# Performance work log

Hardware: AMD Instinct MI355X
Metric: run time of the kernel (lower is better)

Reference implementation:

```python
import jax, jax.numpy as jnp
from jax import lax
import numpy as np


def setup_inputs() -> dict:
    key = jax.random.key(0)
    ks = jax.random.split(key, 7)
    B, C, L, H, K = 64, 256, 2048, 8, 3
    return {
        "src": jax.random.normal(ks[0], (B, C, L), dtype=jnp.float32),
        "conv_w": jax.random.normal(ks[1], (H, C, K), dtype=jnp.float32) * 0.05,
        "conv_b": jax.random.normal(ks[2], (H,), dtype=jnp.float32) * 0.05,
        "bn_gamma": jnp.ones((H,), dtype=jnp.float32),
        "bn_beta": jnp.zeros((H,), dtype=jnp.float32),
        "comb_w": jax.random.normal(ks[5], (H,), dtype=jnp.float32) * 0.3,
        "comb_b": jax.random.normal(ks[6], (1,), dtype=jnp.float32) * 0.05,
        "k": 64,
    }


def reference(src, conv_w, conv_b, bn_gamma, bn_beta, comb_w, comb_b, k):
    # src: (B, C, L); conv_w: (H, C, K)
    B, C, L = src.shape
    H, _, K = conv_w.shape
    # att_conv: valid 1D conv -> (B, H, Lp), Lp = L - K + 1
    xi = lax.conv_general_dilated(src, conv_w, (1,), 'VALID',
                                  dimension_numbers=('NCH', 'OIH', 'NCH'))
    xi = xi + conv_b[None, :, None]
    # BatchNorm1d in the original runs on a batch of 1 (training mode), so
    # stats are per-sample over the length dim; biased var, eps = 1e-5.
    mu = jnp.mean(xi, axis=2, keepdims=True)
    var = jnp.var(xi, axis=2, keepdims=True)
    xn = (xi - mu) * lax.rsqrt(var + 1e-5) * bn_gamma[None, :, None] + bn_beta[None, :, None]
    Lp = xn.shape[2]
    # per-(b, h) top-k indicator; indices are detached (.data) in the original
    _, idx = lax.top_k(xn, k)  # (B, H, k)
    bidx = jnp.arange(B)[:, None, None]
    hidx = jnp.arange(H)[None, :, None]
    ind = jnp.zeros_like(xn).at[bidx, hidx, idx].set(1.0)  # (B, H, Lp)
    m = jax.nn.sigmoid(xn) * ind  # softmask, (B, H, Lp)
    # kernel_size-way shifted-padding sum: M[b,h,l] = sum_i m[b,h,l-i] -> (B, H, L)
    M = sum(jnp.pad(m, ((0, 0), (0, 0), (i, K - 1 - i))) for i in range(K))
    # combine_conv is a 1x1 conv over heads; since softmasked_src[h,c,l] =
    # src[c,l] * M[h,l] / K, the head mix commutes with the src broadcast:
    gate = jnp.einsum('h,bhl->bl', comb_w, M) / K  # (B, L)
    return src * gate[:, None, :] + comb_b[0]  # (B, C, L)
```

## Files before the change

### kernel.cpp

```cpp
#include <hip/hip_runtime.h>
#include <hip/hip_bf16.h>

#define NB 64
#define NC 256
#define NL 2048
#define NH 8
#define KW 3
#define LP (NL - KW + 1)
#define NCHUNK 8
#define CPC (NC / NCHUNK)

typedef float v4f __attribute__((ext_vector_type(4)));

__device__ __forceinline__ unsigned fkey(float x) {
  unsigned b = __float_as_uint(x);
  return (b & 0x80000000u) ? ~b : (b | 0x80000000u);
}

__global__ __launch_bounds__(256) void conv_partial(
    const float* __restrict__ src, const float* __restrict__ conv_w,
    float* __restrict__ part) {
  const int t = threadIdx.x;
  const int lane = t & 63;
  const int l0 = blockIdx.x * 1024 + t * 4;
  const int b = blockIdx.y;
  const int cc = blockIdx.z;
  const int c0 = cc * CPC;

  float acc[NH][4];
#pragma unroll
  for (int h = 0; h < NH; ++h)
#pragma unroll
    for (int j = 0; j < 4; ++j) acc[h][j] = 0.f;

  const float* sp = src + ((size_t)b * NC + c0) * NL + l0;
  const bool tail = (lane == 63) && (l0 + 5 < NL);
#pragma unroll 2
  for (int c = 0; c < CPC; ++c) {
    v4f v = *(const v4f*)sp;
    float e0 = 0.f, e1 = 0.f;
    if (tail) { e0 = sp[4]; e1 = sp[5]; }
    sp += NL;
    float n0 = __shfl_down(v.x, 1);
    float n1 = __shfl_down(v.y, 1);
    if (lane == 63) { n0 = e0; n1 = e1; }
    float s0 = v.x, s1 = v.y, s2 = v.z, s3 = v.w, s4 = n0, s5 = n1;
#pragma unroll
    for (int h = 0; h < NH; ++h) {
      const float* w = conv_w + (h * NC + c0 + c) * KW;
      const float w0 = w[0], w1 = w[1], w2 = w[2];
      acc[h][0] = fmaf(s0, w0, fmaf(s1, w1, fmaf(s2, w2, acc[h][0])));
      acc[h][1] = fmaf(s1, w0, fmaf(s2, w1, fmaf(s3, w2, acc[h][1])));
      acc[h][2] = fmaf(s2, w0, fmaf(s3, w1, fmaf(s4, w2, acc[h][2])));
      acc[h][3] = fmaf(s3, w0, fmaf(s4, w1, fmaf(s5, w2, acc[h][3])));
    }
  }
#pragma unroll
  for (int h = 0; h < NH; ++h) {
    float* pr = part + ((size_t)(b * NH + h) * NCHUNK + cc) * NL + l0;
    if (l0 + 3 < LP) {
      *(v4f*)pr = *(v4f*)acc[h];
    } else {
#pragma unroll
      for (int j = 0; j < 4; ++j)
        if (l0 + j < LP) pr[j] = acc[h][j];
    }
  }
}

__global__ __launch_bounds__(256) void select_block(
    const float* __restrict__ part, float* __restrict__ xi,
    const float* __restrict__ conv_b, const float* __restrict__ bn_gamma,
    const float* __restrict__ bn_beta, const float* __restrict__ comb_w,
    const int* __restrict__ kptr) {
  const int t = threadIdx.x;
  const int lane = t & 63, wid = t >> 6;
  const int bh = blockIdx.x;
  const int h = bh & (NH - 1);
  __shared__ float xs[LP];
  __shared__ float smp[NL + 2];
  __shared__ int hist[256];
  __shared__ float rs[8];
  __shared__ float fbc[2];
  __shared__ int irs[8];
  __shared__ int ibc[4];

  const float cb = conv_b[h];
  const float* p0 = part + (size_t)bh * NCHUNK * NL;
  float s1 = 0.f, s2 = 0.f;
  for (int i = t; i < LP; i += 256) {
    float v0 = p0[i]           + p0[i + NL];
    float v1 = p0[i + 2 * NL]  + p0[i + 3 * NL];
    float v2 = p0[i + 4 * NL]  + p0[i + 5 * NL];
    float v3 = p0[i + 6 * NL]  + p0[i + 7 * NL];
    float v = ((v0 + v1) + (v2 + v3)) + cb;
    xs[i] = v;
    s1 += v;
    s2 += v * v;
  }
#pragma unroll
  for (int off = 32; off > 0; off >>= 1) {
    s1 += __shfl_down(s1, off);
    s2 += __shfl_down(s2, off);
  }
  if (lane == 0) { rs[wid] = s1; rs[wid + 4] = s2; }
  __syncthreads();
  if (t == 0) {
    float S = rs[0] + rs[1] + rs[2] + rs[3];
    float Q = rs[4] + rs[5] + rs[6] + rs[7];
    float mu = S / (float)LP;
    float var = Q / (float)LP - mu * mu;
    float inv = rsqrtf(var + 1e-5f);
    float sc = bn_gamma[h] * inv;
    fbc[0] = sc;
    fbc[1] = bn_beta[h] - mu * sc;
  }
  __syncthreads();
  {
    const float sc = fbc[0], sh = fbc[1];
    for (int i = t; i < LP; i += 256) xs[i] = fmaf(xs[i], sc, sh);
  }
  int kk = kptr[0];
  const int ktot = kk;
  unsigned prefix = 0, pm = 0;
  for (int pass = 0; pass < 4; ++pass) {
    const int shift = 24 - 8 * pass;
    hist[t] = 0;
    __syncthreads();
    for (int i = t; i < LP; i += 256) {
      unsigned u = fkey(xs[i]);
      if ((u & pm) == prefix) atomicAdd(&hist[(u >> shift) & 255], 1);
    }
    __syncthreads();
    if (t < 64) {
      const int h0 = hist[t * 4 + 0], h1 = hist[t * 4 + 1];
      const int h2 = hist[t * 4 + 2], h3 = hist[t * 4 + 3];
      const int g = h0 + h1 + h2 + h3;
      int sfx = g;
#pragma unroll
      for (int off = 1; off < 64; off <<= 1) {
        int o = __shfl(sfx, (t + off) & 63);
        if (t + off < 64) sfx += o;
      }
      const int A = sfx - g;
      const int s3 = A + h3, s2i = s3 + h2, s1i = s2i + h1, s0i = s1i + h0;
      int mybin = -1, mykk = 0;
      if (s0i >= kk && s0i - h0 < kk) { mybin = t * 4 + 0; mykk = kk - (s0i - h0); }
      if (s1i >= kk && s1i - h1 < kk) { mybin = t * 4 + 1; mykk = kk - (s1i - h1); }
      if (s2i >= kk && s2i - h2 < kk) { mybin = t * 4 + 2; mykk = kk - (s2i - h2); }
      if (s3  >= kk && s3  - h3 < kk) { mybin = t * 4 + 3; mykk = kk - (s3 - h3); }
      if (mybin >= 0) { ibc[0] = mybin; ibc[1] = mykk; }
    }
    __syncthreads();
    prefix |= ((unsigned)ibc[0]) << shift;
    pm |= 255u << shift;
    kk = ibc[1];
  }
  const unsigned T = prefix;

  int cgt = 0, ceq = 0;
  for (int i = t; i < LP; i += 256) {
    unsigned u = fkey(xs[i]);
    cgt += (u > T);
    ceq += (u == T);
  }
#pragma unroll
  for (int off = 32; off > 0; off >>= 1) {
    cgt += __shfl_down(cgt, off);
    ceq += __shfl_down(ceq, off);
  }
  if (lane == 0) { irs[wid] = cgt; irs[wid + 4] = ceq; }
  __syncthreads();
  if (t == 0) {
    ibc[2] = irs[0] + irs[1] + irs[2] + irs[3];
    ibc[3] = irs[4] + irs[5] + irs[6] + irs[7];
  }
  __syncthreads();
  const int need_eq = ktot - ibc[2];
  const bool tie = (ibc[3] != need_eq);

  for (int i = t; i < LP; i += 256) {
    float x = xs[i];
    unsigned u = fkey(x);
    bool sel = tie ? (u > T) : (u >= T);
    smp[i + 2] = sel ? 1.f / (1.f + __expf(-x)) : 0.f;
  }
  if (t < 2) { smp[t] = 0.f; smp[NL + t] = 0.f; }
  __syncthreads();
  if (tie && t == 0) {
    int taken = 0;
    for (int i = 0; i < LP && taken < need_eq; ++i) {
      float x = xs[i];
      if (fkey(x) == T) { smp[i + 2] = 1.f / (1.f + __expf(-x)); ++taken; }
    }
  }
  __syncthreads();

  const float cw = comb_w[h] * (1.0f / (float)KW);
  float* row = xi + (size_t)bh * NL;
  for (int l = t; l < NL; l += 256)
    row[l] = cw * ((smp[l + 2] + smp[l + 1]) + smp[l]);
}

__global__ __launch_bounds__(256) void scale_gate(
    const float* __restrict__ src, const float* __restrict__ xi,
    const float* __restrict__ comb_b, float* __restrict__ out) {
  const int t = threadIdx.x;
  const int cchunk = blockIdx.x >> 7;
  const int pairidx = (blockIdx.x & 127) * 256 + t;
  const int b = pairidx >> 9;
  const int l4 = pairidx & 511;
  const float cb = comb_b[0];

  const v4f* xp = (const v4f*)(xi + (size_t)b * NH * NL) + l4;
  v4f g = xp[0];
#pragma unroll
  for (int h = 1; h < NH; ++h) g += xp[(size_t)h * (NL / 4)];

  const int c0 = cchunk * (NC / 16);
  const v4f* sp = (const v4f*)src + ((size_t)b * NC + c0) * (NL / 4) + l4;
  v4f* op = (v4f*)out + ((size_t)b * NC + c0) * (NL / 4) + l4;
#pragma unroll 4
  for (int c = 0; c < NC / 16; ++c) {
    v4f sv = sp[(size_t)c * (NL / 4)];
    v4f ov;
    ov.x = fmaf(sv.x, g.x, cb);
    ov.y = fmaf(sv.y, g.y, cb);
    ov.z = fmaf(sv.z, g.z, cb);
    ov.w = fmaf(sv.w, g.w, cb);
    __builtin_nontemporal_store(ov, op + (size_t)c * (NL / 4));
  }
}

extern "C" void kernel_launch(void* const* d_in, const int* in_sizes, int n_in,
                              void* d_out, int out_size, void* d_ws, size_t ws_size,
                              hipStream_t stream) {
  const float* src = (const float*)d_in[0];
  const float* conv_w = (const float*)d_in[1];
  const float* conv_b = (const float*)d_in[2];
  const float* bn_gamma = (const float*)d_in[3];
  const float* bn_beta = (const float*)d_in[4];
  const float* comb_w = (const float*)d_in[5];
  const float* comb_b = (const float*)d_in[6];
  const int* kptr = (const int*)d_in[7];
  float* out = (float*)d_out;

  float* xi = (float*)d_ws;
  float* part = out;

  conv_partial<<<dim3(2, NB, NCHUNK), 256, 0, stream>>>(src, conv_w, part);
  select_block<<<NB * NH, 256, 0, stream>>>(part, xi, conv_b, bn_gamma,
                                            bn_beta, comb_w, kptr);
  scale_gate<<<2048, 256, 0, stream>>>(src, xi, comb_b, out);
}
```

Baseline: 92.67 us.

## Split conv reduction into more channel chunks and load halo via overlapping vectors

Doubles the number of channel chunks in the partial conv kernel, so twice as many blocks are launched and each does half the channel loop. The cross-lane shuffle used for the two-element halo is replaced by an overlapping, misaligned float4 load. The loop now handles two channels per iteration. The cost is twice as much partial-sum traffic, written by the conv kernel and read back by the select kernel.

```diff
diff --git a/kernel.cpp b/kernel.cpp
--- a/kernel.cpp
+++ b/kernel.cpp
@@ -7,7 +7,7 @@
 #define NH 8
 #define KW 3
 #define LP (NL - KW + 1)
-#define NCHUNK 8
+#define NCHUNK 16
 #define CPC (NC / NCHUNK)
 
 typedef float v4f __attribute__((ext_vector_type(4)));
@@ -21,7 +21,6 @@
     const float* __restrict__ src, const float* __restrict__ conv_w,
     float* __restrict__ part) {
   const int t = threadIdx.x;
-  const int lane = t & 63;
   const int l0 = blockIdx.x * 1024 + t * 4;
   const int b = blockIdx.y;
   const int cc = blockIdx.z;
@@ -33,26 +32,29 @@
 #pragma unroll
     for (int j = 0; j < 4; ++j) acc[h][j] = 0.f;
 
+  const int off2 = (l0 + 5 < NL) ? 2 : 0;
   const float* sp = src + ((size_t)b * NC + c0) * NL + l0;
-  const bool tail = (lane == 63) && (l0 + 5 < NL);
+
 #pragma unroll 2
-  for (int c = 0; c < CPC; ++c) {
-    v4f v = *(const v4f*)sp;
-    float e0 = 0.f, e1 = 0.f;
-    if (tail) { e0 = sp[4]; e1 = sp[5]; }
-    sp += NL;
-    float n0 = __shfl_down(v.x, 1);
-    float n1 = __shfl_down(v.y, 1);
-    if (lane == 63) { n0 = e0; n1 = e1; }
-    float s0 = v.x, s1 = v.y, s2 = v.z, s3 = v.w, s4 = n0, s5 = n1;
+  for (int c = 0; c < CPC; c += 2) {
+    v4f a1 = *(const v4f*)sp;
+    v4f a2 = *(const v4f*)(sp + off2);
+    v4f b1 = *(const v4f*)(sp + NL);
+    v4f b2 = *(const v4f*)(sp + NL + off2);
+    sp += 2 * NL;
 #pragma unroll
     for (int h = 0; h < NH; ++h) {
       const float* w = conv_w + (h * NC + c0 + c) * KW;
       const float w0 = w[0], w1 = w[1], w2 = w[2];
-      acc[h][0] = fmaf(s0, w0, fmaf(s1, w1, fmaf(s2, w2, acc[h][0])));
-      acc[h][1] = fmaf(s1, w0, fmaf(s2, w1, fmaf(s3, w2, acc[h][1])));
-      acc[h][2] = fmaf(s2, w0, fmaf(s3, w1, fmaf(s4, w2, acc[h][2])));
-      acc[h][3] = fmaf(s3, w0, fmaf(s4, w1, fmaf(s5, w2, acc[h][3])));
+      const float w3 = w[3], w4 = w[4], w5 = w[5];
+      acc[h][0] = fmaf(a1.x, w0, fmaf(a1.y, w1, fmaf(a1.z, w2, acc[h][0])));
+      acc[h][1] = fmaf(a1.y, w0, fmaf(a1.z, w1, fmaf(a1.w, w2, acc[h][1])));
+      acc[h][2] = fmaf(a1.z, w0, fmaf(a1.w, w1, fmaf(a2.z, w2, acc[h][2])));
+      acc[h][3] = fmaf(a1.w, w0, fmaf(a2.z, w1, fmaf(a2.w, w2, acc[h][3])));
+      acc[h][0] = fmaf(b1.x, w3, fmaf(b1.y, w4, fmaf(b1.z, w5, acc[h][0])));
+      acc[h][1] = fmaf(b1.y, w3, fmaf(b1.z, w4, fmaf(b1.w, w5, acc[h][1])));
+      acc[h][2] = fmaf(b1.z, w3, fmaf(b1.w, w4, fmaf(b2.z, w5, acc[h][2])));
+      acc[h][3] = fmaf(b1.w, w3, fmaf(b2.z, w4, fmaf(b2.w, w5, acc[h][3])));
     }
   }
 #pragma unroll
@@ -89,11 +91,11 @@
   const float* p0 = part + (size_t)bh * NCHUNK * NL;
   float s1 = 0.f, s2 = 0.f;
   for (int i = t; i < LP; i += 256) {
-    float v0 = p0[i]           + p0[i + NL];
-    float v1 = p0[i + 2 * NL]  + p0[i + 3 * NL];
-    float v2 = p0[i + 4 * NL]  + p0[i + 5 * NL];
-    float v3 = p0[i + 6 * NL]  + p0[i + 7 * NL];
-    float v = ((v0 + v1) + (v2 + v3)) + cb;
+    float v = cb;
+#pragma unroll
+    for (int k = 0; k < NCHUNK; k += 4)
+      v += ((p0[i + (size_t)k * NL] + p0[i + (size_t)(k + 1) * NL]) +
+            (p0[i + (size_t)(k + 2) * NL] + p0[i + (size_t)(k + 3) * NL]));
     xs[i] = v;
     s1 += v;
     s2 += v * v;
```

New measurement: 100.7 us. +8.6%, slower.

## Widen conv tile to 8 outputs per thread and double channel chunks

Applied to the files above, without the earlier changes.

Each conv thread now computes 8 consecutive outputs per head from two vector loads plus a 2-element halo load, replacing the cross-lane shuffle halo exchange. One block covers a full row, and the channel dimension is split into 16 chunks instead of 8. The grid keeps its size while per-thread work and register pressure double (64 accumulators). The partial-sum buffer doubles, so the select kernel reads 16 partials per position instead of 8.

```diff
diff --git a/kernel.cpp b/kernel.cpp
--- a/kernel.cpp
+++ b/kernel.cpp
@@ -7,10 +7,11 @@
 #define NH 8
 #define KW 3
 #define LP (NL - KW + 1)
-#define NCHUNK 8
+#define NCHUNK 16
 #define CPC (NC / NCHUNK)
 
 typedef float v4f __attribute__((ext_vector_type(4)));
+typedef float v2f __attribute__((ext_vector_type(2)));
 
 __device__ __forceinline__ unsigned fkey(float x) {
   unsigned b = __float_as_uint(x);
@@ -21,30 +22,29 @@
     const float* __restrict__ src, const float* __restrict__ conv_w,
     float* __restrict__ part) {
   const int t = threadIdx.x;
-  const int lane = t & 63;
-  const int l0 = blockIdx.x * 1024 + t * 4;
-  const int b = blockIdx.y;
-  const int cc = blockIdx.z;
+  const int l0 = t * 8;
+  const int b = blockIdx.x;
+  const int cc = blockIdx.y;
   const int c0 = cc * CPC;
 
-  float acc[NH][4];
+  float acc[NH][8];
 #pragma unroll
   for (int h = 0; h < NH; ++h)
 #pragma unroll
-    for (int j = 0; j < 4; ++j) acc[h][j] = 0.f;
+    for (int j = 0; j < 8; ++j) acc[h][j] = 0.f;
 
   const float* sp = src + ((size_t)b * NC + c0) * NL + l0;
-  const bool tail = (lane == 63) && (l0 + 5 < NL);
+  const bool has8 = (l0 + 9 < NL);
 #pragma unroll 2
   for (int c = 0; c < CPC; ++c) {
-    v4f v = *(const v4f*)sp;
+    v4f A = *(const v4f*)sp;
+    v4f B = *(const v4f*)(sp + 4);
     float e0 = 0.f, e1 = 0.f;
-    if (tail) { e0 = sp[4]; e1 = sp[5]; }
+    if (has8) { v2f E = *(const v2f*)(sp + 8); e0 = E.x; e1 = E.y; }
     sp += NL;
-    float n0 = __shfl_down(v.x, 1);
-    float n1 = __shfl_down(v.y, 1);
-    if (lane == 63) { n0 = e0; n1 = e1; }
-    float s0 = v.x, s1 = v.y, s2 = v.z, s3 = v.w, s4 = n0, s5 = n1;
+    const float s0 = A.x, s1 = A.y, s2 = A.z, s3 = A.w;
+    const float s4 = B.x, s5 = B.y, s6 = B.z, s7 = B.w;
+    const float s8 = e0, s9 = e1;
 #pragma unroll
     for (int h = 0; h < NH; ++h) {
       const float* w = conv_w + (h * NC + c0 + c) * KW;
@@ -53,16 +53,21 @@
       acc[h][1] = fmaf(s1, w0, fmaf(s2, w1, fmaf(s3, w2, acc[h][1])));
       acc[h][2] = fmaf(s2, w0, fmaf(s3, w1, fmaf(s4, w2, acc[h][2])));
       acc[h][3] = fmaf(s3, w0, fmaf(s4, w1, fmaf(s5, w2, acc[h][3])));
+      acc[h][4] = fmaf(s4, w0, fmaf(s5, w1, fmaf(s6, w2, acc[h][4])));
+      acc[h][5] = fmaf(s5, w0, fmaf(s6, w1, fmaf(s7, w2, acc[h][5])));
+      acc[h][6] = fmaf(s6, w0, fmaf(s7, w1, fmaf(s8, w2, acc[h][6])));
+      acc[h][7] = fmaf(s7, w0, fmaf(s8, w1, fmaf(s9, w2, acc[h][7])));
     }
   }
 #pragma unroll
   for (int h = 0; h < NH; ++h) {
     float* pr = part + ((size_t)(b * NH + h) * NCHUNK + cc) * NL + l0;
-    if (l0 + 3 < LP) {
-      *(v4f*)pr = *(v4f*)acc[h];
+    if (l0 + 7 < LP) {
+      *(v4f*)pr = *(v4f*)&acc[h][0];
+      *(v4f*)(pr + 4) = *(v4f*)&acc[h][4];
     } else {
 #pragma unroll
-      for (int j = 0; j < 4; ++j)
+      for (int j = 0; j < 8; ++j)
         if (l0 + j < LP) pr[j] = acc[h][j];
     }
   }
@@ -89,11 +94,11 @@
   const float* p0 = part + (size_t)bh * NCHUNK * NL;
   float s1 = 0.f, s2 = 0.f;
   for (int i = t; i < LP; i += 256) {
-    float v0 = p0[i]           + p0[i + NL];
-    float v1 = p0[i + 2 * NL]  + p0[i + 3 * NL];
-    float v2 = p0[i + 4 * NL]  + p0[i + 5 * NL];
-    float v3 = p0[i + 6 * NL]  + p0[i + 7 * NL];
-    float v = ((v0 + v1) + (v2 + v3)) + cb;
+    float v = cb;
+#pragma unroll
+    for (int k = 0; k < NCHUNK; k += 4)
+      v += ((p0[i + (size_t)k * NL] + p0[i + (size_t)(k + 1) * NL]) +
+            (p0[i + (size_t)(k + 2) * NL] + p0[i + (size_t)(k + 3) * NL]));
     xs[i] = v;
     s1 += v;
     s2 += v * v;
@@ -248,7 +253,7 @@
   float* xi = (float*)d_ws;
   float* part = out;
 
-  conv_partial<<<dim3(2, NB, NCHUNK), 256, 0, stream>>>(src, conv_w, part);
+  conv_partial<<<dim3(NB, NCHUNK), 256, 0, stream>>>(src, conv_w, part);
   select_block<<<NB * NH, 256, 0, stream>>>(part, xi, conv_b, bn_gamma,
                                             bn_beta, comb_w, kptr);
   scale_gate<<<2048, 256, 0, stream>>>(src, xi, comb_b, out);
```

After: 100.4 us. +8.4%, slower.

## Replace channel-chunked conv partials with direct per-tile conv and LDS reduction

Applied to the files above, without the earlier changes.

The conv kernel no longer splits channels into 8 chunks written as partial sums to global memory. Each block now covers a 128-wide L tile of one batch, with two channel halves reduced through LDS, and it writes the biased conv output straight to xi. The select kernel then reads one row instead of summing 8 partials, which removes a large global write and read round trip. In exchange each thread computes only one output per loaded value, so per-load FMA work and weight reuse drop, and it uses scalar loads and two shuffles per channel.

```diff
diff --git a/kernel.cpp b/kernel.cpp
--- a/kernel.cpp
+++ b/kernel.cpp
@@ -7,8 +7,6 @@
 #define NH 8
 #define KW 3
 #define LP (NL - KW + 1)
-#define NCHUNK 8
-#define CPC (NC / NCHUNK)
 
 typedef float v4f __attribute__((ext_vector_type(4)));
 
@@ -17,60 +15,58 @@
   return (b & 0x80000000u) ? ~b : (b | 0x80000000u);
 }
 
-__global__ __launch_bounds__(256) void conv_partial(
+__global__ __launch_bounds__(256) void conv_direct(
     const float* __restrict__ src, const float* __restrict__ conv_w,
-    float* __restrict__ part) {
+    const float* __restrict__ conv_b, float* __restrict__ xi) {
   const int t = threadIdx.x;
   const int lane = t & 63;
-  const int l0 = blockIdx.x * 1024 + t * 4;
+  const int wv = t >> 6;
+  const int lrow = wv & 1;
+  const int c0 = __builtin_amdgcn_readfirstlane((wv >> 1) * 128);
+  const int l0 = blockIdx.x * 128;
   const int b = blockIdx.y;
-  const int cc = blockIdx.z;
-  const int c0 = cc * CPC;
-
-  float acc[NH][4];
-#pragma unroll
-  for (int h = 0; h < NH; ++h)
-#pragma unroll
-    for (int j = 0; j < 4; ++j) acc[h][j] = 0.f;
-
-  const float* sp = src + ((size_t)b * NC + c0) * NL + l0;
-  const bool tail = (lane == 63) && (l0 + 5 < NL);
-#pragma unroll 2
-  for (int c = 0; c < CPC; ++c) {
-    v4f v = *(const v4f*)sp;
-    float e0 = 0.f, e1 = 0.f;
-    if (tail) { e0 = sp[4]; e1 = sp[5]; }
+  const int l = l0 + lrow * 64 + lane;
+
+  __shared__ float plds[2][NH][128];
+
+  float acc[NH];
+#pragma unroll
+  for (int h = 0; h < NH; ++h) acc[h] = 0.f;
+
+  const float* sp = src + ((size_t)b * NC + c0) * NL + l;
+  const bool in1 = (l + 1 < NL), in2 = (l + 2 < NL);
+#pragma unroll 4
+  for (int c = 0; c < NC / 2; ++c) {
+    float v = *sp;
+    float n1 = __shfl_down(v, 1);
+    float n2 = __shfl_down(v, 2);
+    if (lane >= 62) {
+      n2 = in2 ? sp[2] : 0.f;
+      if (lane == 63) n1 = in1 ? sp[1] : 0.f;
+    }
     sp += NL;
-    float n0 = __shfl_down(v.x, 1);
-    float n1 = __shfl_down(v.y, 1);
-    if (lane == 63) { n0 = e0; n1 = e1; }
-    float s0 = v.x, s1 = v.y, s2 = v.z, s3 = v.w, s4 = n0, s5 = n1;
 #pragma unroll
     for (int h = 0; h < NH; ++h) {
-      const float* w = conv_w + (h * NC + c0 + c) * KW;
-      const float w0 = w[0], w1 = w[1], w2 = w[2];
-      acc[h][0] = fmaf(s0, w0, fmaf(s1, w1, fmaf(s2, w2, acc[h][0])));
-      acc[h][1] = fmaf(s1, w0, fmaf(s2, w1, fmaf(s3, w2, acc[h][1])));
-      acc[h][2] = fmaf(s2, w0, fmaf(s3, w1, fmaf(s4, w2, acc[h][2])));
-      acc[h][3] = fmaf(s3, w0, fmaf(s4, w1, fmaf(s5, w2, acc[h][3])));
-    }
-  }
-#pragma unroll
-  for (int h = 0; h < NH; ++h) {
-    float* pr = part + ((size_t)(b * NH + h) * NCHUNK + cc) * NL + l0;
-    if (l0 + 3 < LP) {
-      *(v4f*)pr = *(v4f*)acc[h];
-    } else {
-#pragma unroll
-      for (int j = 0; j < 4; ++j)
-        if (l0 + j < LP) pr[j] = acc[h][j];
-    }
+      const float* wp = conv_w + (h * NC + c0 + c) * KW;
+      acc[h] = fmaf(v, wp[0], fmaf(n1, wp[1], fmaf(n2, wp[2], acc[h])));
+    }
+  }
+#pragma unroll
+  for (int h = 0; h < NH; ++h) plds[wv >> 1][h][lrow * 64 + lane] = acc[h];
+  __syncthreads();
+#pragma unroll
+  for (int q = 0; q < 4; ++q) {
+    const int i = q * 256 + t;
+    const int h = i >> 7, ll = i & 127;
+    const int lg = l0 + ll;
+    if (lg < LP)
+      xi[((size_t)b * NH + h) * NL + lg] =
+          (plds[0][h][ll] + plds[1][h][ll]) + conv_b[h];
   }
 }
 
 __global__ __launch_bounds__(256) void select_block(
-    const float* __restrict__ part, float* __restrict__ xi,
-    const float* __restrict__ conv_b, const float* __restrict__ bn_gamma,
+    float* __restrict__ xi, const float* __restrict__ bn_gamma,
     const float* __restrict__ bn_beta, const float* __restrict__ comb_w,
     const int* __restrict__ kptr) {
   const int t = threadIdx.x;
@@ -85,15 +81,10 @@
   __shared__ int irs[8];
   __shared__ int ibc[4];
 
-  const float cb = conv_b[h];
-  const float* p0 = part + (size_t)bh * NCHUNK * NL;
+  float* row = xi + (size_t)bh * NL;
   float s1 = 0.f, s2 = 0.f;
   for (int i = t; i < LP; i += 256) {
-    float v0 = p0[i]           + p0[i + NL];
-    float v1 = p0[i + 2 * NL]  + p0[i + 3 * NL];
-    float v2 = p0[i + 4 * NL]  + p0[i + 5 * NL];
-    float v3 = p0[i + 6 * NL]  + p0[i + 7 * NL];
-    float v = ((v0 + v1) + (v2 + v3)) + cb;
+    float v = row[i];
     xs[i] = v;
     s1 += v;
     s2 += v * v;
@@ -197,7 +188,6 @@
   __syncthreads();
 
   const float cw = comb_w[h] * (1.0f / (float)KW);
-  float* row = xi + (size_t)bh * NL;
   for (int l = t; l < NL; l += 256)
     row[l] = cw * ((smp[l + 2] + smp[l + 1]) + smp[l]);
 }
@@ -246,10 +236,8 @@
   float* out = (float*)d_out;
 
   float* xi = (float*)d_ws;
-  float* part = out;
-
-  conv_partial<<<dim3(2, NB, NCHUNK), 256, 0, stream>>>(src, conv_w, part);
-  select_block<<<NB * NH, 256, 0, stream>>>(part, xi, conv_b, bn_gamma,
-                                            bn_beta, comb_w, kptr);
+
+  conv_direct<<<dim3(NL / 128, NB), 256, 0, stream>>>(src, conv_w, conv_b, xi);
+  select_block<<<NB * NH, 256, 0, stream>>>(xi, bn_gamma, bn_beta, comb_w, kptr);
   scale_gate<<<2048, 256, 0, stream>>>(src, xi, comb_b, out);
 }
```

Result: slower. 127.9 us (+38.0%).
